# Kernel optimization log

Hardware: AMD Instinct MI355X
Metric: run time of the kernel (lower is better)

Reference implementation:

```python
import jax, jax.numpy as jnp
import numpy as np
from jax import lax

B = 32
NUM_CLASSES = 80
NUM_ANCHORS = 3
IMG_SIZE = 320
STRIDES = (8, 16, 32)
TOPK = 1000
CONF_THRESH = 0.05
NMS_THRESH = 0.6
EPS = 1e-10

ANCHOR_SIZES = np.array([[16, 16], [32, 32], [64, 48],
                         [64, 64], [96, 96], [128, 96],
                         [128, 128], [192, 160], [256, 256]],
                        dtype=np.float32).reshape(3, NUM_ANCHORS, 2)


def _build_anchors():
    # mirrors YOWOv3.generate_anchors
    boxes, strides = [], []
    for lvl, s in enumerate(STRIDES):
        f = IMG_SIZE // s
        ys, xs = np.meshgrid(np.arange(f), np.arange(f), indexing='ij')
        xy = np.stack([xs, ys], axis=-1).astype(np.float32).reshape(-1, 1, 2)
        xy = np.repeat(xy, NUM_ANCHORS, axis=1) * s            # [f*f, A, 2]
        wh = np.broadcast_to(ANCHOR_SIZES[lvl], (f * f, NUM_ANCHORS, 2))
        boxes.append(np.concatenate([xy, wh], axis=-1).reshape(-1, 4))
        strides.append(np.full(f * f * NUM_ANCHORS, s, dtype=np.float32))
    return np.concatenate(boxes, 0), np.concatenate(strides, 0)


def setup_inputs() -> dict:
    key = jax.random.key(0)
    k1, k2, k3 = jax.random.split(key, 3)
    anchors_np, stride_np = _build_anchors()
    M = anchors_np.shape[0]  # 6300
    conf_pred = jax.random.normal(k1, (B, M, 1), dtype=jnp.float32)
    cls_pred = jax.random.normal(k2, (B, M, NUM_CLASSES), dtype=jnp.float32) * 2.0
    reg_pred = jax.random.normal(k3, (B, M, 4), dtype=jnp.float32) * 0.5
    return {
        'conf_pred': conf_pred,
        'cls_pred': cls_pred,
        'reg_pred': reg_pred,
        'anchors': jnp.asarray(anchors_np),
        'stride_map': jnp.asarray(stride_np),
    }


def _decode_boxes(anchors, stride_map, reg_pred):
    # anchors [M,4] (cx, cy, w, h) in pixels; reg_pred [B,M,4]
    ctr = anchors[None, :, :2] + jax.nn.sigmoid(reg_pred[..., :2]) * stride_map[None, :, None]
    wh = anchors[None, :, 2:] * jnp.exp(reg_pred[..., 2:])
    return jnp.concatenate([ctr - 0.5 * wh, ctr + 0.5 * wh], axis=-1)  # [B,M,4] x1y1x2y2


def _nms_keep(boxes, scores, labels):
    # boxes [K,4] sorted by descending score; per-class greedy NMS -> bool keep [K]
    x1, y1, x2, y2 = boxes[:, 0], boxes[:, 1], boxes[:, 2], boxes[:, 3]
    areas = (x2 - x1) * (y2 - y1)
    xx1 = jnp.maximum(x1[:, None], x1[None, :])
    yy1 = jnp.maximum(y1[:, None], y1[None, :])
    xx2 = jnp.minimum(x2[:, None], x2[None, :])
    yy2 = jnp.minimum(y2[:, None], y2[None, :])
    inter = jnp.maximum(EPS, xx2 - xx1) * jnp.maximum(EPS, yy2 - yy1)
    union = jnp.maximum(areas[:, None] + areas[None, :] - inter, EPS)
    iou = inter / union
    suppress = (iou > NMS_THRESH) & (labels[:, None] == labels[None, :])
    keep0 = scores >= CONF_THRESH
    idxs = jnp.arange(boxes.shape[0])

    def body(i, keep):
        # if box i is kept, suppress all later same-class boxes with iou > thresh
        return keep & ~(keep[i] & suppress[i] & (idxs > i))

    return lax.fori_loop(0, boxes.shape[0], body, keep0)


def reference(conf_pred, cls_pred, reg_pred, anchors, stride_map):
    box_pred = _decode_boxes(anchors, stride_map, reg_pred)              # [B,M,4]
    joint = jax.nn.sigmoid(conf_pred) * jax.nn.softmax(cls_pred, -1)     # [B,M,C]
    scores = jnp.max(joint, axis=-1)                                     # [B,M]
    labels = jnp.argmax(joint, axis=-1)                                  # [B,M]

    top_scores, top_idx = lax.top_k(scores, TOPK)                        # sorted desc
    top_labels = jnp.take_along_axis(labels, top_idx, axis=1)
    top_boxes = jnp.take_along_axis(box_pred, top_idx[..., None], axis=1)
    top_boxes = jnp.clip(top_boxes / IMG_SIZE, 0.0, 1.0)                 # [B,K,4]

    keep = jax.vmap(_nms_keep)(top_boxes, top_scores, top_labels)        # [B,K] bool
    return top_scores, top_labels, top_boxes, keep
```

## Files before the change

### kernel.cpp

```cpp
#include <hip/hip_runtime.h>
#include <stdint.h>

#define NB 32
#define NM 6300
#define NC 80
#define NTOP 1000
#define NPAD 1024
#define NCAND 2048
#define NBINS 4096
#define BDT 1024

static constexpr float IMGSZ   = 320.0f;
static constexpr float CONF_TH = 0.05f;
static constexpr float NMS_TH  = 0.6f;
static constexpr float EPSF    = 1e-10f;

static constexpr size_t OFF_SCORES = 0;
static constexpr size_t OFF_LABELS = OFF_SCORES + (size_t)NB * NM * 4;
static constexpr size_t OFF_TIDX   = OFF_LABELS + (size_t)NB * NM * 4;
static constexpr size_t OFF_NBOX   = OFF_TIDX   + (size_t)NB * NPAD * 4;
static constexpr size_t OFF_NLAB   = OFF_NBOX   + (size_t)NB * NPAD * 16;
static constexpr size_t OFF_SUP    = ((OFF_NLAB + (size_t)NB * NPAD * 4) + 1023) & ~(size_t)1023;

__global__ __launch_bounds__(256) void k_score(const float* __restrict__ conf,
                                               const float* __restrict__ cls,
                                               float* __restrict__ scores,
                                               int* __restrict__ labels) {
#pragma clang fp contract(off)
    int t = blockIdx.x * blockDim.x + threadIdx.x;
    int a = t >> 4;
    int l = t & 15;
    if (a >= NB * NM) return;
    const float* row = cls + (size_t)a * NC;

    float v[5];
#pragma unroll
    for (int k = 0; k < 5; ++k) v[k] = row[l + 16 * k];

    float bv = v[0];
    int bi = l;
#pragma unroll
    for (int k = 1; k < 5; ++k) {
        int c = l + 16 * k;
        if (v[k] > bv) { bv = v[k]; bi = c; }
    }
#pragma unroll
    for (int m = 1; m < 16; m <<= 1) {
        float ov = __shfl_xor(bv, m, 16);
        int   oi = __shfl_xor(bi, m, 16);
        if (ov > bv || (ov == bv && oi < bi)) { bv = ov; bi = oi; }
    }
    float s = 0.0f;
#pragma unroll
    for (int k = 0; k < 5; ++k) s += expf(v[k] - bv);
#pragma unroll
    for (int m = 1; m < 16; m <<= 1) s += __shfl_xor(s, m, 16);

    if (l == 0) {
        float cf  = conf[a];
        float sig = 1.0f / (1.0f + expf(-cf));
        float inv = 1.0f / s;
        scores[a] = sig * inv;
        labels[a] = bi;
    }
}

__global__ __launch_bounds__(BDT) void k_topk(const float* __restrict__ scores,
                                              float* __restrict__ out_scores,
                                              int* __restrict__ top_idx) {
    __shared__ uint32_t hist[NBINS];
    __shared__ uint64_t key[NCAND];
    __shared__ int scnt;
    __shared__ int sT;
    int b = blockIdx.x, tid = threadIdx.x;
    const float* sb = scores + (size_t)b * NM;

    for (int i = tid; i < NBINS; i += BDT) hist[i] = 0;
    for (int i = tid; i < NCAND; i += BDT) key[i] = 0;
    if (tid == 0) scnt = 0;
    __syncthreads();

    for (int i = tid; i < NM; i += BDT)
        atomicAdd(&hist[__float_as_uint(sb[i]) >> 20], 1u);
    __syncthreads();

    if (tid < 64) {
        int l = tid;
        uint32_t q = 0;
        for (int i = 0; i < 64; ++i) q += hist[l * 64 + i];
        uint32_t s = q;
        for (int off = 1; off < 64; off <<= 1) {
            uint32_t o = __shfl_down(s, off);
            if (l + off < 64) s += o;
        }
        uint64_t m = __ballot(s >= (uint32_t)NTOP);
        int c = 63 - __clzll(m);
        uint32_t sc_ = __shfl(s, c);
        uint32_t qc  = __shfl(q, c);
        uint32_t tail = sc_ - qc;
        uint32_t v = hist[c * 64 + l];
        uint32_t s2 = v;
        for (int off = 1; off < 64; off <<= 1) {
            uint32_t o = __shfl_down(s2, off);
            if (l + off < 64) s2 += o;
        }
        uint64_t m2 = __ballot(s2 + tail >= (uint32_t)NTOP);
        int T = c * 64 + (63 - __clzll(m2));
        if (l == 0) sT = T;
    }
    __syncthreads();

    uint32_t T = (uint32_t)sT;
    int lane = tid & 63;
    for (int i = tid; i < NM; i += BDT) {
        uint32_t bits = __float_as_uint(sb[i]);
        bool pred = (bits >> 20) >= T;
        uint64_t mask = __ballot(pred);
        if (pred) {
            int leader = __ffsll((unsigned long long)mask) - 1;
            int prefix = __popcll(mask & ((1ull << lane) - 1));
            int base = 0;
            if (lane == leader) base = atomicAdd(&scnt, (int)__popcll(mask));
            base = __shfl(base, leader);
            int pos = base + prefix;
            if (pos < NCAND)
                key[pos] = ((uint64_t)bits << 32) | (uint32_t)(~(uint32_t)i);
        }
    }
    __syncthreads();

    for (int kk = 2; kk <= NCAND; kk <<= 1) {
        for (int j = kk >> 1; j > 0; j >>= 1) {
            for (int t = tid; t < NCAND / 2; t += BDT) {
                int i   = 2 * t - (t & (j - 1));
                int ixj = i + j;
                uint64_t a = key[i], c2 = key[ixj];
                bool up = (i & kk) == 0;
                if (up ? (a < c2) : (a > c2)) { key[i] = c2; key[ixj] = a; }
            }
            __syncthreads();
        }
    }

    for (int r = tid; r < NTOP; r += BDT) {
        uint64_t kk2 = key[r];
        out_scores[b * NTOP + r] = __uint_as_float((uint32_t)(kk2 >> 32));
        top_idx[b * NPAD + r]    = (int)(~(uint32_t)kk2);
    }
}

__global__ __launch_bounds__(256) void k_decode(const int* __restrict__ top_idx,
                                                const int* __restrict__ labels,
                                                const float* __restrict__ reg,
                                                const float* __restrict__ anchors,
                                                const float* __restrict__ stridemap,
                                                float* __restrict__ out_labels,
                                                float* __restrict__ out_boxes,
                                                float* __restrict__ nbox,
                                                int* __restrict__ nlab) {
#pragma clang fp contract(off)
    int t = blockIdx.x * blockDim.x + threadIdx.x;
    if (t >= NB * NTOP) return;
    int b = t / NTOP, r = t % NTOP;
    int idx = top_idx[b * NPAD + r];
    int lab = labels[(size_t)b * NM + idx];
    out_labels[b * NTOP + r] = (float)lab;

    const float* rg = reg + ((size_t)b * NM + idx) * 4;
    float rx = rg[0], ry = rg[1], rw = rg[2], rh = rg[3];
    const float* an = anchors + (size_t)idx * 4;
    float ax = an[0], ay = an[1], aw = an[2], ah = an[3];
    float st = stridemap[idx];

    float sx = 1.0f / (1.0f + expf(-rx));
    float sy = 1.0f / (1.0f + expf(-ry));
    float cx = ax + sx * st;
    float cy = ay + sy * st;
    float w  = aw * expf(rw);
    float h  = ah * expf(rh);
    float x1 = cx - 0.5f * w, y1 = cy - 0.5f * h;
    float x2 = cx + 0.5f * w, y2 = cy + 0.5f * h;

    float nx1 = fminf(fmaxf(x1 / IMGSZ, 0.0f), 1.0f);
    float ny1 = fminf(fmaxf(y1 / IMGSZ, 0.0f), 1.0f);
    float nx2 = fminf(fmaxf(x2 / IMGSZ, 0.0f), 1.0f);
    float ny2 = fminf(fmaxf(y2 / IMGSZ, 0.0f), 1.0f);

    float4 bx = make_float4(nx1, ny1, nx2, ny2);
    ((float4*)out_boxes)[b * NTOP + r] = bx;
    ((float4*)nbox)[b * NPAD + r]      = bx;
    nlab[b * NPAD + r] = lab;
}

__global__ __launch_bounds__(64) void k_supmat(const float* __restrict__ nbox,
                                               const int* __restrict__ nlab,
                                               uint64_t* __restrict__ sup) {
#pragma clang fp contract(off)
    int b  = blockIdx.y;
    int bx = blockIdx.x;
    int t  = bx >> 1;
    int h  = bx & 1;
    int tj = (int)((sqrtf(8.0f * (float)t + 1.0f) - 1.0f) * 0.5f);
    while ((tj + 1) * (tj + 2) / 2 <= t) ++tj;
    while (tj * (tj + 1) / 2 > t) --tj;
    int ti = t - tj * (tj + 1) / 2;

    int lane = threadIdx.x;
    int i = ti * 64 + lane;
    int j = tj * 64 + lane;

    float4 bi = ((const float4*)nbox)[b * NPAD + i];
    float  ai = (bi.z - bi.x) * (bi.w - bi.y);
    int    li = nlab[b * NPAD + i];
    float4 bj = ((const float4*)nbox)[b * NPAD + j];
    float  aj = (bj.z - bj.x) * (bj.w - bj.y);
    int    lj = nlab[b * NPAD + j];
    bool ivalid = (i < NTOP);

    uint64_t mybits = 0;
#pragma unroll 8
    for (int u = 0; u < 32; ++u) {
        int jj = h * 32 + u;
        float bjx = __shfl(bj.x, jj);
        float bjy = __shfl(bj.y, jj);
        float bjz = __shfl(bj.z, jj);
        float bjw = __shfl(bj.w, jj);
        float ajv = __shfl(aj, jj);
        int   ljv = __shfl(lj, jj);
        int   jg  = tj * 64 + jj;
        float xx1 = fmaxf(bi.x, bjx);
        float yy1 = fmaxf(bi.y, bjy);
        float xx2 = fminf(bi.z, bjz);
        float yy2 = fminf(bi.w, bjw);
        float inter = fmaxf(EPSF, xx2 - xx1) * fmaxf(EPSF, yy2 - yy1);
        float uni   = fmaxf(ai + ajv - inter, EPSF);
        float iou   = inter / uni;
        bool sup_ij = (i < jg) && ivalid && (jg < NTOP) &&
                      (li == ljv) && (iou > NMS_TH);
        uint64_t bal = __ballot(sup_ij);
        if (lane == jj) mybits = bal;
    }
    if ((lane >> 5) == h)
        sup[(((size_t)b * 16 + tj) * 16 + ti) * 64 + lane] = mybits;
}

__global__ __launch_bounds__(1024) void k_nms(const float* __restrict__ out_scores,
                                              const uint64_t* __restrict__ sup,
                                              float* __restrict__ out_keep) {
    __shared__ uint64_t Kw[16];
    int b    = blockIdx.x;
    int w    = threadIdx.x >> 6;
    int lane = threadIdx.x & 63;
    const uint64_t* supb = sup + (size_t)b * 16 * 16 * 64;

    uint64_t wrow[16];
#pragma unroll
    for (int ti = 0; ti < 16; ++ti)
        wrow[ti] = (ti <= w) ? supb[((size_t)w * 16 + ti) * 64 + lane] : 0ULL;

    int pos = w * 64 + lane;
    bool k0 = (pos < NTOP) && (out_scores[b * NTOP + pos] >= CONF_TH);

    uint64_t ext = 0;
#pragma unroll
    for (int s = 0; s < 16; ++s) {
        if (w == s) {
            bool cand = k0 && (ext == 0ULL);
            uint64_t wself = wrow[s];
            uint64_t alive = __ballot(cand);
            for (int it = 0; it < 64; ++it) {
                bool dead = (wself & alive) != 0ULL;
                uint64_t na = __ballot(cand && !dead);
                if (na == alive) break;
                alive = na;
            }
            if (lane == 0) Kw[s] = alive;
            if (pos < NTOP)
                out_keep[b * NTOP + pos] = ((alive >> lane) & 1ULL) ? 1.0f : 0.0f;
        }
        __syncthreads();
        if (w > s) ext |= wrow[s] & Kw[s];
    }
}

extern "C" void kernel_launch(void* const* d_in, const int* in_sizes, int n_in,
                              void* d_out, int out_size, void* d_ws, size_t ws_size,
                              hipStream_t stream) {
    const float* conf = (const float*)d_in[0];
    const float* cls  = (const float*)d_in[1];
    const float* reg  = (const float*)d_in[2];
    const float* anch = (const float*)d_in[3];
    const float* strm = (const float*)d_in[4];

    float* out        = (float*)d_out;
    float* out_scores = out;
    float* out_labels = out + NB * NTOP;
    float* out_boxes  = out + 2 * NB * NTOP;
    float* out_keep   = out + 2 * NB * NTOP + NB * NTOP * 4;

    char* ws = (char*)d_ws;
    float*    scores = (float*)(ws + OFF_SCORES);
    int*      labels = (int*)(ws + OFF_LABELS);
    int*      tidx   = (int*)(ws + OFF_TIDX);
    float*    nbox   = (float*)(ws + OFF_NBOX);
    int*      nlab   = (int*)(ws + OFF_NLAB);
    uint64_t* sup    = (uint64_t*)(ws + OFF_SUP);

    k_score<<<(NB * NM * 16) / 256, 256, 0, stream>>>(conf, cls, scores, labels);
    k_topk<<<NB, BDT, 0, stream>>>(scores, out_scores, tidx);
    k_decode<<<(NB * NTOP + 255) / 256, 256, 0, stream>>>(tidx, labels, reg, anch, strm,
                                                          out_labels, out_boxes, nbox, nlab);
    k_supmat<<<dim3(272, NB), 64, 0, stream>>>(nbox, nlab, sup);
    k_nms<<<NB, 1024, 0, stream>>>(out_scores, sup, out_keep);
}
```

Measured before the change: 70.88 us.

## Register/shuffle bitonic sort, fuse decode into topk, restructure supmat to one block per tile

```diff
diff --git a/kernel.cpp b/kernel.cpp
--- a/kernel.cpp
+++ b/kernel.cpp
@@ -17,8 +17,7 @@
 
 static constexpr size_t OFF_SCORES = 0;
 static constexpr size_t OFF_LABELS = OFF_SCORES + (size_t)NB * NM * 4;
-static constexpr size_t OFF_TIDX   = OFF_LABELS + (size_t)NB * NM * 4;
-static constexpr size_t OFF_NBOX   = OFF_TIDX   + (size_t)NB * NPAD * 4;
+static constexpr size_t OFF_NBOX   = OFF_LABELS + (size_t)NB * NM * 4;
 static constexpr size_t OFF_NLAB   = OFF_NBOX   + (size_t)NB * NPAD * 16;
 static constexpr size_t OFF_SUP    = ((OFF_NLAB + (size_t)NB * NPAD * 4) + 1023) & ~(size_t)1023;
 
@@ -66,8 +65,16 @@
 }
 
 __global__ __launch_bounds__(BDT) void k_topk(const float* __restrict__ scores,
+                                              const int* __restrict__ labels,
+                                              const float* __restrict__ reg,
+                                              const float* __restrict__ anchors,
+                                              const float* __restrict__ stridemap,
                                               float* __restrict__ out_scores,
-                                              int* __restrict__ top_idx) {
+                                              float* __restrict__ out_labels,
+                                              float* __restrict__ out_boxes,
+                                              float* __restrict__ nbox,
+                                              int* __restrict__ nlab) {
+#pragma clang fp contract(off)
     __shared__ uint32_t hist[NBINS];
     __shared__ uint64_t key[NCAND];
     __shared__ int scnt;
@@ -129,119 +136,120 @@
     }
     __syncthreads();
 
+    uint64_t e0 = key[tid];
+    uint64_t e1 = key[tid + 1024];
+
+#pragma unroll
     for (int kk = 2; kk <= NCAND; kk <<= 1) {
+#pragma unroll
         for (int j = kk >> 1; j > 0; j >>= 1) {
-            for (int t = tid; t < NCAND / 2; t += BDT) {
-                int i   = 2 * t - (t & (j - 1));
-                int ixj = i + j;
-                uint64_t a = key[i], c2 = key[ixj];
-                bool up = (i & kk) == 0;
-                if (up ? (a < c2) : (a > c2)) { key[i] = c2; key[ixj] = a; }
+            if (j == 1024) {
+                uint64_t mx = (e0 >= e1) ? e0 : e1;
+                uint64_t mn = (e0 >= e1) ? e1 : e0;
+                e0 = mx; e1 = mn;
+            } else if (j >= 64) {
+                __syncthreads();
+                key[tid] = e0; key[tid + 1024] = e1;
+                __syncthreads();
+                uint64_t o0 = key[tid ^ j];
+                uint64_t o1 = key[(tid + 1024) ^ j];
+                bool lo  = ((tid & j) == 0);
+                bool up0 = ((tid & kk) == 0);
+                bool up1 = (((tid + 1024) & kk) == 0);
+                e0 = (lo == up0) ? ((e0 >= o0) ? e0 : o0) : ((e0 >= o0) ? o0 : e0);
+                e1 = (lo == up1) ? ((e1 >= o1) ? e1 : o1) : ((e1 >= o1) ? o1 : e1);
+            } else {
+                uint64_t o0 = __shfl_xor((unsigned long long)e0, j);
+                uint64_t o1 = __shfl_xor((unsigned long long)e1, j);
+                bool lo  = ((lane & j) == 0);
+                bool up0 = ((tid & kk) == 0);
+                bool up1 = (((tid + 1024) & kk) == 0);
+                e0 = (lo == up0) ? ((e0 >= o0) ? e0 : o0) : ((e0 >= o0) ? o0 : e0);
+                e1 = (lo == up1) ? ((e1 >= o1) ? e1 : o1) : ((e1 >= o1) ? o1 : e1);
             }
-            __syncthreads();
-        }
-    }
-
-    for (int r = tid; r < NTOP; r += BDT) {
-        uint64_t kk2 = key[r];
-        out_scores[b * NTOP + r] = __uint_as_float((uint32_t)(kk2 >> 32));
-        top_idx[b * NPAD + r]    = (int)(~(uint32_t)kk2);
-    }
-}
-
-__global__ __launch_bounds__(256) void k_decode(const int* __restrict__ top_idx,
-                                                const int* __restrict__ labels,
-                                                const float* __restrict__ reg,
-                                                const float* __restrict__ anchors,
-                                                const float* __restrict__ stridemap,
-                                                float* __restrict__ out_labels,
-                                                float* __restrict__ out_boxes,
-                                                float* __restrict__ nbox,
-                                                int* __restrict__ nlab) {
-#pragma clang fp contract(off)
-    int t = blockIdx.x * blockDim.x + threadIdx.x;
-    if (t >= NB * NTOP) return;
-    int b = t / NTOP, r = t % NTOP;
-    int idx = top_idx[b * NPAD + r];
-    int lab = labels[(size_t)b * NM + idx];
-    out_labels[b * NTOP + r] = (float)lab;
-
-    const float* rg = reg + ((size_t)b * NM + idx) * 4;
-    float rx = rg[0], ry = rg[1], rw = rg[2], rh = rg[3];
-    const float* an = anchors + (size_t)idx * 4;
-    float ax = an[0], ay = an[1], aw = an[2], ah = an[3];
-    float st = stridemap[idx];
-
-    float sx = 1.0f / (1.0f + expf(-rx));
-    float sy = 1.0f / (1.0f + expf(-ry));
-    float cx = ax + sx * st;
-    float cy = ay + sy * st;
-    float w  = aw * expf(rw);
-    float h  = ah * expf(rh);
-    float x1 = cx - 0.5f * w, y1 = cy - 0.5f * h;
-    float x2 = cx + 0.5f * w, y2 = cy + 0.5f * h;
-
-    float nx1 = fminf(fmaxf(x1 / IMGSZ, 0.0f), 1.0f);
-    float ny1 = fminf(fmaxf(y1 / IMGSZ, 0.0f), 1.0f);
-    float nx2 = fminf(fmaxf(x2 / IMGSZ, 0.0f), 1.0f);
-    float ny2 = fminf(fmaxf(y2 / IMGSZ, 0.0f), 1.0f);
-
-    float4 bx = make_float4(nx1, ny1, nx2, ny2);
-    ((float4*)out_boxes)[b * NTOP + r] = bx;
-    ((float4*)nbox)[b * NPAD + r]      = bx;
-    nlab[b * NPAD + r] = lab;
+        }
+    }
+
+    if (tid < NTOP) {
+        uint32_t sbits = (uint32_t)(e0 >> 32);
+        int idx = (int)(~(uint32_t)e0);
+        out_scores[b * NTOP + tid] = __uint_as_float(sbits);
+        int lab = labels[(size_t)b * NM + idx];
+        out_labels[b * NTOP + tid] = (float)lab;
+
+        const float* rg = reg + ((size_t)b * NM + idx) * 4;
+        float rx = rg[0], ry = rg[1], rw = rg[2], rh = rg[3];
+        const float* an = anchors + (size_t)idx * 4;
+        float ax = an[0], ay = an[1], aw = an[2], ah = an[3];
+        float st = stridemap[idx];
+
+        float sx = 1.0f / (1.0f + expf(-rx));
+        float sy = 1.0f / (1.0f + expf(-ry));
+        float cx = ax + sx * st;
+        float cy = ay + sy * st;
+        float w  = aw * expf(rw);
+        float h  = ah * expf(rh);
+        float x1 = cx - 0.5f * w, y1 = cy - 0.5f * h;
+        float x2 = cx + 0.5f * w, y2 = cy + 0.5f * h;
+
+        float nx1 = fminf(fmaxf(x1 / IMGSZ, 0.0f), 1.0f);
+        float ny1 = fminf(fmaxf(y1 / IMGSZ, 0.0f), 1.0f);
+        float nx2 = fminf(fmaxf(x2 / IMGSZ, 0.0f), 1.0f);
+        float ny2 = fminf(fmaxf(y2 / IMGSZ, 0.0f), 1.0f);
+
+        float4 bx = make_float4(nx1, ny1, nx2, ny2);
+        ((float4*)out_boxes)[b * NTOP + tid] = bx;
+        ((float4*)nbox)[b * NPAD + tid]      = bx;
+        nlab[b * NPAD + tid] = lab;
+    }
 }
 
 __global__ __launch_bounds__(64) void k_supmat(const float* __restrict__ nbox,
                                                const int* __restrict__ nlab,
                                                uint64_t* __restrict__ sup) {
 #pragma clang fp contract(off)
-    int b  = blockIdx.y;
-    int bx = blockIdx.x;
-    int t  = bx >> 1;
-    int h  = bx & 1;
+    int b = blockIdx.y;
+    int t = blockIdx.x;
     int tj = (int)((sqrtf(8.0f * (float)t + 1.0f) - 1.0f) * 0.5f);
     while ((tj + 1) * (tj + 2) / 2 <= t) ++tj;
     while (tj * (tj + 1) / 2 > t) --tj;
     int ti = t - tj * (tj + 1) / 2;
 
     int lane = threadIdx.x;
-    int i = ti * 64 + lane;
     int j = tj * 64 + lane;
 
-    float4 bi = ((const float4*)nbox)[b * NPAD + i];
-    float  ai = (bi.z - bi.x) * (bi.w - bi.y);
-    int    li = nlab[b * NPAD + i];
-    float4 bj = ((const float4*)nbox)[b * NPAD + j];
-    float  aj = (bj.z - bj.x) * (bj.w - bj.y);
+    float4 cj = ((const float4*)nbox)[b * NPAD + j];
+    float  aj = (cj.z - cj.x) * (cj.w - cj.y);
     int    lj = nlab[b * NPAD + j];
-    bool ivalid = (i < NTOP);
-
-    uint64_t mybits = 0;
-#pragma unroll 8
-    for (int u = 0; u < 32; ++u) {
-        int jj = h * 32 + u;
-        float bjx = __shfl(bj.x, jj);
-        float bjy = __shfl(bj.y, jj);
-        float bjz = __shfl(bj.z, jj);
-        float bjw = __shfl(bj.w, jj);
-        float ajv = __shfl(aj, jj);
-        int   ljv = __shfl(lj, jj);
-        int   jg  = tj * 64 + jj;
-        float xx1 = fmaxf(bi.x, bjx);
-        float yy1 = fmaxf(bi.y, bjy);
-        float xx2 = fminf(bi.z, bjz);
-        float yy2 = fminf(bi.w, bjw);
+    bool   jv = (j < NTOP);
+
+    float4 ri = ((const float4*)nbox)[b * NPAD + ti * 64 + lane];
+    float  ar = (ri.z - ri.x) * (ri.w - ri.y);
+    int    rl = nlab[b * NPAD + ti * 64 + lane];
+
+    uint32_t lobits = 0, hibits = 0;
+#pragma unroll
+    for (int ii = 0; ii < 64; ++ii) {
+        float bix = __shfl(ri.x, ii);
+        float biy = __shfl(ri.y, ii);
+        float biz = __shfl(ri.z, ii);
+        float biw = __shfl(ri.w, ii);
+        float aiv = __shfl(ar,   ii);
+        int   liv = __shfl(rl,   ii);
+        int   ig  = ti * 64 + ii;
+        float xx1 = fmaxf(bix, cj.x);
+        float yy1 = fmaxf(biy, cj.y);
+        float xx2 = fminf(biz, cj.z);
+        float yy2 = fminf(biw, cj.w);
         float inter = fmaxf(EPSF, xx2 - xx1) * fmaxf(EPSF, yy2 - yy1);
-        float uni   = fmaxf(ai + ajv - inter, EPSF);
+        float uni   = fmaxf(aiv + aj - inter, EPSF);
         float iou   = inter / uni;
-        bool sup_ij = (i < jg) && ivalid && (jg < NTOP) &&
-                      (li == ljv) && (iou > NMS_TH);
-        uint64_t bal = __ballot(sup_ij);
-        if (lane == jj) mybits = bal;
-    }
-    if ((lane >> 5) == h)
-        sup[(((size_t)b * 16 + tj) * 16 + ti) * 64 + lane] = mybits;
+        bool pred = (ig < j) && (ig < NTOP) && jv && (liv == lj) && (iou > NMS_TH);
+        if (ii < 32) lobits |= (pred ? (1u << ii) : 0u);
+        else         hibits |= (pred ? (1u << (ii - 32)) : 0u);
+    }
+    sup[(((size_t)b * 16 + tj) * 16 + ti) * 64 + lane] =
+        ((uint64_t)hibits << 32) | (uint64_t)lobits;
 }
 
 __global__ __launch_bounds__(1024) void k_nms(const float* __restrict__ out_scores,
@@ -301,15 +309,13 @@
     char* ws = (char*)d_ws;
     float*    scores = (float*)(ws + OFF_SCORES);
     int*      labels = (int*)(ws + OFF_LABELS);
-    int*      tidx   = (int*)(ws + OFF_TIDX);
     float*    nbox   = (float*)(ws + OFF_NBOX);
     int*      nlab   = (int*)(ws + OFF_NLAB);
     uint64_t* sup    = (uint64_t*)(ws + OFF_SUP);
 
     k_score<<<(NB * NM * 16) / 256, 256, 0, stream>>>(conf, cls, scores, labels);
-    k_topk<<<NB, BDT, 0, stream>>>(scores, out_scores, tidx);
-    k_decode<<<(NB * NTOP + 255) / 256, 256, 0, stream>>>(tidx, labels, reg, anch, strm,
-                                                          out_labels, out_boxes, nbox, nlab);
-    k_supmat<<<dim3(272, NB), 64, 0, stream>>>(nbox, nlab, sup);
+    k_topk<<<NB, BDT, 0, stream>>>(scores, labels, reg, anch, strm,
+                                   out_scores, out_labels, out_boxes, nbox, nlab);
+    k_supmat<<<dim3(136, NB), 64, 0, stream>>>(nbox, nlab, sup);
     k_nms<<<NB, 1024, 0, stream>>>(out_scores, sup, out_keep);
 }
```

Measured after the change: 73.58 us. +3.8%, slower.

## Replace bitonic sort with rank-by-counting in topk, widen supmat blocks

Applied to the files above, without the earlier changes.

```diff
diff --git a/kernel.cpp b/kernel.cpp
--- a/kernel.cpp
+++ b/kernel.cpp
@@ -8,7 +8,6 @@
 #define NPAD 1024
 #define NCAND 2048
 #define NBINS 4096
-#define BDT 1024
 
 static constexpr float IMGSZ   = 320.0f;
 static constexpr float CONF_TH = 0.05f;
@@ -65,22 +64,21 @@
     }
 }
 
-__global__ __launch_bounds__(BDT) void k_topk(const float* __restrict__ scores,
-                                              float* __restrict__ out_scores,
-                                              int* __restrict__ top_idx) {
+__global__ __launch_bounds__(1024) void k_topk(const float* __restrict__ scores,
+                                               float* __restrict__ out_scores,
+                                               int* __restrict__ top_idx) {
     __shared__ uint32_t hist[NBINS];
-    __shared__ uint64_t key[NCAND];
-    __shared__ int scnt;
-    __shared__ int sT;
+    __shared__ __align__(16) uint64_t key[NCAND];
+    __shared__ int sT, scnt;
     int b = blockIdx.x, tid = threadIdx.x;
     const float* sb = scores + (size_t)b * NM;
 
-    for (int i = tid; i < NBINS; i += BDT) hist[i] = 0;
-    for (int i = tid; i < NCAND; i += BDT) key[i] = 0;
+    for (int i = tid; i < NBINS; i += 1024) hist[i] = 0;
+    for (int i = tid; i < NCAND; i += 1024) key[i] = 0;
     if (tid == 0) scnt = 0;
     __syncthreads();
 
-    for (int i = tid; i < NM; i += BDT)
+    for (int i = tid; i < NM; i += 1024)
         atomicAdd(&hist[__float_as_uint(sb[i]) >> 20], 1u);
     __syncthreads();
 
@@ -112,7 +110,7 @@
 
     uint32_t T = (uint32_t)sT;
     int lane = tid & 63;
-    for (int i = tid; i < NM; i += BDT) {
+    for (int i = tid; i < NM; i += 1024) {
         uint32_t bits = __float_as_uint(sb[i]);
         bool pred = (bits >> 20) >= T;
         uint64_t mask = __ballot(pred);
@@ -129,23 +127,21 @@
     }
     __syncthreads();
 
-    for (int kk = 2; kk <= NCAND; kk <<= 1) {
-        for (int j = kk >> 1; j > 0; j >>= 1) {
-            for (int t = tid; t < NCAND / 2; t += BDT) {
-                int i   = 2 * t - (t & (j - 1));
-                int ixj = i + j;
-                uint64_t a = key[i], c2 = key[ixj];
-                bool up = (i & kk) == 0;
-                if (up ? (a < c2) : (a > c2)) { key[i] = c2; key[ixj] = a; }
-            }
-            __syncthreads();
-        }
-    }
-
-    for (int r = tid; r < NTOP; r += BDT) {
-        uint64_t kk2 = key[r];
-        out_scores[b * NTOP + r] = __uint_as_float((uint32_t)(kk2 >> 32));
-        top_idx[b * NPAD + r]    = (int)(~(uint32_t)kk2);
+    int C = scnt; if (C > NCAND) C = NCAND;
+    int C2 = (C + 1) >> 1;
+    const ulonglong2* k2 = (const ulonglong2*)key;
+    for (int t = tid; t < C; t += 1024) {
+        uint64_t kt = key[t];
+        uint32_t rank = 0;
+        for (int j = 0; j < C2; ++j) {
+            ulonglong2 kk = k2[j];
+            rank += (kk.x > kt) ? 1u : 0u;
+            rank += (kk.y > kt) ? 1u : 0u;
+        }
+        if (rank < (uint32_t)NTOP) {
+            out_scores[b * NTOP + rank] = __uint_as_float((uint32_t)(kt >> 32));
+            top_idx[b * NPAD + rank]    = (int)(~(uint32_t)kt);
+        }
     }
 }
 
@@ -192,20 +188,20 @@
     nlab[b * NPAD + r] = lab;
 }
 
-__global__ __launch_bounds__(64) void k_supmat(const float* __restrict__ nbox,
-                                               const int* __restrict__ nlab,
-                                               uint64_t* __restrict__ sup) {
+__global__ __launch_bounds__(256) void k_supmat(const float* __restrict__ nbox,
+                                                const int* __restrict__ nlab,
+                                                uint64_t* __restrict__ sup) {
 #pragma clang fp contract(off)
-    int b  = blockIdx.y;
-    int bx = blockIdx.x;
-    int t  = bx >> 1;
-    int h  = bx & 1;
+    int b = blockIdx.y;
+    int t = blockIdx.x;
     int tj = (int)((sqrtf(8.0f * (float)t + 1.0f) - 1.0f) * 0.5f);
     while ((tj + 1) * (tj + 2) / 2 <= t) ++tj;
     while (tj * (tj + 1) / 2 > t) --tj;
     int ti = t - tj * (tj + 1) / 2;
 
-    int lane = threadIdx.x;
+    int lane = threadIdx.x & 63;
+    int w    = threadIdx.x >> 6;
+
     int i = ti * 64 + lane;
     int j = tj * 64 + lane;
 
@@ -213,20 +209,19 @@
     float  ai = (bi.z - bi.x) * (bi.w - bi.y);
     int    li = nlab[b * NPAD + i];
     float4 bj = ((const float4*)nbox)[b * NPAD + j];
-    float  aj = (bj.z - bj.x) * (bj.w - bj.y);
     int    lj = nlab[b * NPAD + j];
-    bool ivalid = (i < NTOP);
+    bool   iv = (i < NTOP);
 
     uint64_t mybits = 0;
-#pragma unroll 8
-    for (int u = 0; u < 32; ++u) {
-        int jj = h * 32 + u;
+#pragma unroll
+    for (int u = 0; u < 16; ++u) {
+        int jj = (w << 4) | u;
         float bjx = __shfl(bj.x, jj);
         float bjy = __shfl(bj.y, jj);
         float bjz = __shfl(bj.z, jj);
         float bjw = __shfl(bj.w, jj);
-        float ajv = __shfl(aj, jj);
         int   ljv = __shfl(lj, jj);
+        float ajv = (bjz - bjx) * (bjw - bjy);
         int   jg  = tj * 64 + jj;
         float xx1 = fmaxf(bi.x, bjx);
         float yy1 = fmaxf(bi.y, bjy);
@@ -235,12 +230,11 @@
         float inter = fmaxf(EPSF, xx2 - xx1) * fmaxf(EPSF, yy2 - yy1);
         float uni   = fmaxf(ai + ajv - inter, EPSF);
         float iou   = inter / uni;
-        bool sup_ij = (i < jg) && ivalid && (jg < NTOP) &&
-                      (li == ljv) && (iou > NMS_TH);
-        uint64_t bal = __ballot(sup_ij);
+        bool pred = (i < jg) && iv && (jg < NTOP) && (li == ljv) && (iou > NMS_TH);
+        uint64_t bal = __ballot(pred);
         if (lane == jj) mybits = bal;
     }
-    if ((lane >> 5) == h)
+    if ((lane >> 4) == w)
         sup[(((size_t)b * 16 + tj) * 16 + ti) * 64 + lane] = mybits;
 }
 
@@ -307,9 +301,9 @@
     uint64_t* sup    = (uint64_t*)(ws + OFF_SUP);
 
     k_score<<<(NB * NM * 16) / 256, 256, 0, stream>>>(conf, cls, scores, labels);
-    k_topk<<<NB, BDT, 0, stream>>>(scores, out_scores, tidx);
+    k_topk<<<NB, 1024, 0, stream>>>(scores, out_scores, tidx);
     k_decode<<<(NB * NTOP + 255) / 256, 256, 0, stream>>>(tidx, labels, reg, anch, strm,
                                                           out_labels, out_boxes, nbox, nlab);
-    k_supmat<<<dim3(272, NB), 64, 0, stream>>>(nbox, nlab, sup);
+    k_supmat<<<dim3(136, NB), 256, 0, stream>>>(nbox, nlab, sup);
     k_nms<<<NB, 1024, 0, stream>>>(out_scores, sup, out_keep);
 }
```

Measured after the change: 80.33 us. 1.13x slower.
